# Kernel tuning notes

Hardware: AMD Instinct MI355X
Metric: run time of the kernel (lower is better)

The kernel has to match this reference:

```python
import jax, jax.numpy as jnp
import numpy as np


def setup_inputs() -> dict:
    key = jax.random.key(0)
    k1, k2 = jax.random.split(key)
    N, D, E = 8192, 4096, 16
    x = jax.random.normal(k1, (N, D), dtype=jnp.float32)
    Wg = jax.random.normal(k2, (E, D), dtype=jnp.float32) * (1.0 / np.sqrt(D))
    return {"x": x, "Wg": Wg, "k": 2}


def reference(x, Wg, k):
    # Router logits and gates (fp32, matching input.float() + Linear.float())
    logits = jnp.einsum("nd,ed->ne", x.astype(jnp.float32), Wg)  # [N, E]
    gates = jax.nn.softmax(logits, axis=1)
    N, E = gates.shape

    # top-k expert selection; concat column-wise like torch chunk(k, dim=1)
    _, topk_idx = jax.lax.top_k(gates, k)            # [N, k]
    idx = topk_idx.T.reshape(-1)                     # [k*N] token->expert

    # one-hot masks for each of the k choices, concatenated along token dim
    mask = jax.nn.one_hot(idx, E, dtype=jnp.int32)   # [k*N, E]

    # gate weights for each choice; normalize across the k=2 choices
    w_cols = jnp.take_along_axis(gates, topk_idx, axis=1)  # [N, k]
    w_norm = w_cols[:, 0] + w_cols[:, 1]
    weight = (w_cols / w_norm[:, None]).T.reshape(-1)      # [k*N]

    # expert token counts and within-expert positions (cumsum trick)
    expert_token_count = jnp.sum(mask, axis=0)                       # [E]
    pos_in_expert = jnp.sum((jnp.cumsum(mask, axis=0) - 1) * mask, axis=1)  # [k*N]

    # load-balancing aux loss uses only the top-1 mask
    me = jnp.mean(gates, axis=0)
    ce = jnp.mean(mask[:N].astype(jnp.float32), axis=0)
    l_aux = jnp.sum(me * ce) * E

    # exclusive cumsum of expert counts -> base offset per expert
    expert_offset = jnp.cumsum(expert_token_count) - expert_token_count
    token_pos_after = pos_in_expert + expert_offset[idx]             # [k*N]

    token_num = N * k
    token_pos_before = jnp.zeros((token_num,), dtype=jnp.int32).at[token_pos_after].set(
        jnp.arange(token_num, dtype=jnp.int32)
    )
    return (l_aux, token_pos_after, token_pos_before, expert_token_count, weight)
```

## Files before the change

kernel.cpp:

```cpp
#include <hip/hip_runtime.h>
#include <math.h>

#define N_TOK 8192
#define DIM   4096
#define NE    16
#define TOKS  (2*N_TOK)
#define NCHUNK (TOKS/64)
#define NSEG 4
#define SEGF4 (DIM/4/NSEG)
#define D4 (DIM/4)

#define OUT_LAUX 0
#define OUT_TPA  1
#define OUT_TPB  (1+TOKS)
#define OUT_CNT  (1+2*TOKS)
#define OUT_W    (1+2*TOKS+NE)

__global__ __launch_bounds__(256, 4) void k1_logits(
    const float4* __restrict__ x4, const float4* __restrict__ wg4,
    float* __restrict__ part)
{
    const int lane  = threadIdx.x & 63;
    const int wave  = threadIdx.x >> 6;
    const int gwave = blockIdx.x * 4 + wave;
    const int seg   = gwave & (NSEG - 1);
    const int row0  = (gwave >> 2) * 4;

    float acc[4][NE];
    #pragma unroll
    for (int r = 0; r < 4; ++r)
        #pragma unroll
        for (int e = 0; e < NE; ++e) acc[r][e] = 0.f;

    #pragma unroll 2
    for (int j = 0; j < SEGF4 / 64; ++j) {
        const int col = seg * SEGF4 + j * 64 + lane;
        float4 xv0 = x4[(size_t)(row0 + 0) * D4 + col];
        float4 xv1 = x4[(size_t)(row0 + 1) * D4 + col];
        float4 xv2 = x4[(size_t)(row0 + 2) * D4 + col];
        float4 xv3 = x4[(size_t)(row0 + 3) * D4 + col];
        #pragma unroll
        for (int e = 0; e < NE; ++e) {
            float4 wv = wg4[e * D4 + col];
            acc[0][e] = fmaf(xv0.x, wv.x, acc[0][e]);
            acc[0][e] = fmaf(xv0.y, wv.y, acc[0][e]);
            acc[0][e] = fmaf(xv0.z, wv.z, acc[0][e]);
            acc[0][e] = fmaf(xv0.w, wv.w, acc[0][e]);
            acc[1][e] = fmaf(xv1.x, wv.x, acc[1][e]);
            acc[1][e] = fmaf(xv1.y, wv.y, acc[1][e]);
            acc[1][e] = fmaf(xv1.z, wv.z, acc[1][e]);
            acc[1][e] = fmaf(xv1.w, wv.w, acc[1][e]);
            acc[2][e] = fmaf(xv2.x, wv.x, acc[2][e]);
            acc[2][e] = fmaf(xv2.y, wv.y, acc[2][e]);
            acc[2][e] = fmaf(xv2.z, wv.z, acc[2][e]);
            acc[2][e] = fmaf(xv2.w, wv.w, acc[2][e]);
            acc[3][e] = fmaf(xv3.x, wv.x, acc[3][e]);
            acc[3][e] = fmaf(xv3.y, wv.y, acc[3][e]);
            acc[3][e] = fmaf(xv3.z, wv.z, acc[3][e]);
            acc[3][e] = fmaf(xv3.w, wv.w, acc[3][e]);
        }
    }

    float v[64];
    #pragma unroll
    for (int r = 0; r < 4; ++r)
        #pragma unroll
        for (int e = 0; e < NE; ++e) v[r * 16 + e] = acc[r][e];

    #pragma unroll
    for (int s = 0; s < 6; ++s) {
        const int step = 1 << s;
        const int hi = (lane >> s) & 1;
        #pragma unroll
        for (int i = 0; i < (64 >> (s + 1)); ++i) {
            float a = v[2 * i], b = v[2 * i + 1];
            float mine = hi ? b : a;
            float oth  = hi ? a : b;
            v[i] = mine + __shfl_xor(oth, step);
        }
    }
    part[(size_t)seg * (N_TOK * NE) + (size_t)row0 * NE + lane] = v[0];
}

__global__ __launch_bounds__(256) void k2_route(
    const float* __restrict__ part, int* __restrict__ pr,
    int* __restrict__ hist, float* __restrict__ me_part,
    float* __restrict__ out)
{
    const int row   = blockIdx.x * 256 + threadIdx.x;
    const int lane  = threadIdx.x & 63;
    const int gwave = row >> 6;

    float lg[NE];
    #pragma unroll
    for (int e = 0; e < NE; ++e) lg[e] = 0.f;
    #pragma unroll
    for (int s = 0; s < NSEG; ++s) {
        const float4* p4 = (const float4*)(part + (size_t)s * (N_TOK * NE) + (size_t)row * NE);
        #pragma unroll
        for (int q = 0; q < 4; ++q) {
            float4 t = p4[q];
            lg[q * 4 + 0] += t.x;
            lg[q * 4 + 1] += t.y;
            lg[q * 4 + 2] += t.z;
            lg[q * 4 + 3] += t.w;
        }
    }

    float m1 = -INFINITY; int i1 = 0;
    #pragma unroll
    for (int e = 0; e < NE; ++e)
        if (lg[e] > m1) { m1 = lg[e]; i1 = e; }
    float m2 = -INFINITY; int i2 = 0;
    #pragma unroll
    for (int e = 0; e < NE; ++e)
        if (e != i1 && lg[e] > m2) { m2 = lg[e]; i2 = e; }

    float ssum = 0.f, ex[NE];
    #pragma unroll
    for (int e = 0; e < NE; ++e) { ex[e] = __expf(lg[e] - m1); ssum += ex[e]; }
    const float inv = 1.f / ssum;

    const float e2v = __expf(m2 - m1);
    const float w1  = 1.f / (1.f + e2v);
    out[OUT_W + row]         = w1;
    out[OUT_W + N_TOK + row] = 1.f - w1;

    float mymev = 0.f;
    #pragma unroll
    for (int e = 0; e < NE; ++e) {
        float mv = ex[e] * inv;
        mv += __shfl_xor(mv, 32); mv += __shfl_xor(mv, 16);
        mv += __shfl_xor(mv, 8);  mv += __shfl_xor(mv, 4);
        mv += __shfl_xor(mv, 2);  mv += __shfl_xor(mv, 1);
        if (lane == e) mymev = mv;
    }
    if (lane < NE) me_part[gwave * NE + lane] = mymev;

    const unsigned long long mlt = (1ull << lane) - 1ull;
    int rk1 = 0, rk2 = 0;
    #pragma unroll
    for (int eo = 0; eo < NE; ++eo) {
        unsigned long long mA = __ballot(i1 == eo);
        unsigned long long mB = __ballot(i2 == eo);
        if (i1 == eo) rk1 = (int)__popcll(mA & mlt);
        if (i2 == eo) rk2 = (int)__popcll(mB & mlt);
        if (lane == eo) {
            hist[gwave * NE + eo]                 = (int)__popcll(mA);
            hist[(NCHUNK / 2 + gwave) * NE + eo]  = (int)__popcll(mB);
        }
    }
    pr[row]         = i1 | (rk1 << 8);
    pr[N_TOK + row] = i2 | (rk2 << 8);
}

__global__ __launch_bounds__(1024) void k3_scan(
    const int* __restrict__ hist, const float* __restrict__ me_part,
    int* __restrict__ base, float* __restrict__ out)
{
    __shared__ int   sh[NCHUNK][NE];
    __shared__ int   counts[NE];
    __shared__ int   offs[NE];
    __shared__ int   ce_cnt[NE];
    __shared__ float me_red[64][NE];

    const int tid  = threadIdx.x;
    const int lane = tid & 63;
    const int wave = tid >> 6;

    if (wave < NE) {
        const int ecol = wave;
        int carry = 0;
        #pragma unroll
        for (int cc = 0; cc < 4; ++cc) {
            const int c = cc * 64 + lane;
            int v = hist[c * NE + ecol];
            const int orig = v;
            #pragma unroll
            for (int off = 1; off < 64; off <<= 1) {
                int n = __shfl_up(v, off, 64);
                if (lane >= off) v += n;
            }
            const int excl = v - orig + carry;
            if (c == NCHUNK / 2) ce_cnt[ecol] = excl;
            sh[c][ecol] = excl;
            carry += __shfl(v, 63, 64);
        }
        if (lane == 0) counts[ecol] = carry;
    }
    __syncthreads();

    if (tid == 0) {
        int run = 0;
        for (int e = 0; e < NE; ++e) { offs[e] = run; run += counts[e]; }
    }
    {
        const int e = tid & 15, g = tid >> 4;
        me_red[g][e] = me_part[g * NE + e] + me_part[(g + 64) * NE + e];
    }
    __syncthreads();

    if (wave == 0 && lane < NE) {
        float me = 0.f;
        for (int g = 0; g < 64; ++g) me += me_red[g][lane];
        me *= (1.0f / N_TOK);
        const float ce = (float)ce_cnt[lane] * (1.0f / N_TOK);
        float la = me * ce * (float)NE;
        la += __shfl_xor(la, 8); la += __shfl_xor(la, 4);
        la += __shfl_xor(la, 2); la += __shfl_xor(la, 1);
        if (lane == 0) out[OUT_LAUX] = la;
        out[OUT_CNT + lane] = (float)counts[lane];
    }

    #pragma unroll
    for (int k = 0; k < (NCHUNK * NE) / 1024; ++k) {
        const int i = k * 1024 + tid;
        base[i] = ((const int*)sh)[i] + offs[i & 15];
    }
}

__global__ __launch_bounds__(256) void k4_place(
    const int* __restrict__ pr, const int* __restrict__ base,
    float* __restrict__ out)
{
    const int t  = blockIdx.x * 256 + threadIdx.x;
    const int v  = pr[t];
    const int e  = v & 255;
    const int rk = v >> 8;
    const int c  = t >> 6;
    const int pos = base[c * NE + e] + rk;
    out[OUT_TPA + t]   = (float)pos;
    out[OUT_TPB + pos] = (float)t;
}

extern "C" void kernel_launch(void* const* d_in, const int* in_sizes, int n_in,
                              void* d_out, int out_size, void* d_ws, size_t ws_size,
                              hipStream_t stream) {
    const float* x  = (const float*)d_in[0];
    const float* wg = (const float*)d_in[1];
    float* out = (float*)d_out;

    char* w = (char*)d_ws;
    float* part    = (float*)w;
    w += (size_t)NSEG * N_TOK * NE * sizeof(float);
    int* pr        = (int*)w;   w += TOKS * sizeof(int);
    int* hist      = (int*)w;   w += NCHUNK * NE * sizeof(int);
    int* base      = (int*)w;   w += NCHUNK * NE * sizeof(int);
    float* me_part = (float*)w;

    k1_logits<<<(N_TOK / 4) * NSEG / 4, 256, 0, stream>>>(
        (const float4*)x, (const float4*)wg, part);
    k2_route<<<N_TOK / 256, 256, 0, stream>>>(part, pr, hist, me_part, out);
    k3_scan<<<1, 1024, 0, stream>>>(hist, me_part, base, out);
    k4_place<<<TOKS / 256, 256, 0, stream>>>(pr, base, out);
}
```

Measured before the change: 248.3 us.

## Fuse scan into placement kernel, stagger column order, simplify logits reduction

```diff
diff --git a/kernel.cpp b/kernel.cpp
--- a/kernel.cpp
+++ b/kernel.cpp
@@ -6,9 +6,10 @@
 #define NE    16
 #define TOKS  (2*N_TOK)
 #define NCHUNK (TOKS/64)
-#define NSEG 4
-#define SEGF4 (DIM/4/NSEG)
-#define D4 (DIM/4)
+#define D4    (DIM/4)
+#define NSEG  4
+#define SEGF4 (D4/NSEG)
+#define JITER (SEGF4/64)
 
 #define OUT_LAUX 0
 #define OUT_TPA  1
@@ -16,15 +17,16 @@
 #define OUT_CNT  (1+2*TOKS)
 #define OUT_W    (1+2*TOKS+NE)
 
-__global__ __launch_bounds__(256, 4) void k1_logits(
+__global__ __launch_bounds__(256) void k1_logits(
     const float4* __restrict__ x4, const float4* __restrict__ wg4,
     float* __restrict__ part)
 {
     const int lane  = threadIdx.x & 63;
     const int wave  = threadIdx.x >> 6;
     const int gwave = blockIdx.x * 4 + wave;
-    const int seg   = gwave & (NSEG - 1);
+    const int seg   = gwave & 3;
     const int row0  = (gwave >> 2) * 4;
+    const int ph    = gwave & 3;
 
     float acc[4][NE];
     #pragma unroll
@@ -33,7 +35,8 @@
         for (int e = 0; e < NE; ++e) acc[r][e] = 0.f;
 
     #pragma unroll 2
-    for (int j = 0; j < SEGF4 / 64; ++j) {
+    for (int jj = 0; jj < JITER; ++jj) {
+        const int j   = (jj + ph) & (JITER - 1);
         const int col = seg * SEGF4 + j * 64 + lane;
         float4 xv0 = x4[(size_t)(row0 + 0) * D4 + col];
         float4 xv1 = x4[(size_t)(row0 + 1) * D4 + col];
@@ -41,7 +44,7 @@
         float4 xv3 = x4[(size_t)(row0 + 3) * D4 + col];
         #pragma unroll
         for (int e = 0; e < NE; ++e) {
-            float4 wv = wg4[e * D4 + col];
+            const float4 wv = wg4[e * D4 + col];
             acc[0][e] = fmaf(xv0.x, wv.x, acc[0][e]);
             acc[0][e] = fmaf(xv0.y, wv.y, acc[0][e]);
             acc[0][e] = fmaf(xv0.z, wv.z, acc[0][e]);
@@ -61,45 +64,47 @@
         }
     }
 
-    float v[64];
     #pragma unroll
     for (int r = 0; r < 4; ++r)
         #pragma unroll
-        for (int e = 0; e < NE; ++e) v[r * 16 + e] = acc[r][e];
-
-    #pragma unroll
-    for (int s = 0; s < 6; ++s) {
-        const int step = 1 << s;
-        const int hi = (lane >> s) & 1;
-        #pragma unroll
-        for (int i = 0; i < (64 >> (s + 1)); ++i) {
-            float a = v[2 * i], b = v[2 * i + 1];
-            float mine = hi ? b : a;
-            float oth  = hi ? a : b;
-            v[i] = mine + __shfl_xor(oth, step);
-        }
-    }
-    part[(size_t)seg * (N_TOK * NE) + (size_t)row0 * NE + lane] = v[0];
-}
-
-__global__ __launch_bounds__(256) void k2_route(
+        for (int e = 0; e < NE; ++e) {
+            float v = acc[r][e];
+            v += __shfl_xor(v, 32); v += __shfl_xor(v, 16);
+            v += __shfl_xor(v, 8);  v += __shfl_xor(v, 4);
+            v += __shfl_xor(v, 2);  v += __shfl_xor(v, 1);
+            acc[r][e] = v;
+        }
+
+    if (lane < 4) {
+        const int r = lane;
+        float4* p4 = (float4*)part;
+        const size_t base = ((size_t)seg * N_TOK + row0 + r) * 4;
+        p4[base + 0] = make_float4(acc[r][0],  acc[r][1],  acc[r][2],  acc[r][3]);
+        p4[base + 1] = make_float4(acc[r][4],  acc[r][5],  acc[r][6],  acc[r][7]);
+        p4[base + 2] = make_float4(acc[r][8],  acc[r][9],  acc[r][10], acc[r][11]);
+        p4[base + 3] = make_float4(acc[r][12], acc[r][13], acc[r][14], acc[r][15]);
+    }
+}
+
+__global__ __launch_bounds__(128) void k2_route(
     const float* __restrict__ part, int* __restrict__ pr,
     int* __restrict__ hist, float* __restrict__ me_part,
     float* __restrict__ out)
 {
-    const int row   = blockIdx.x * 256 + threadIdx.x;
+    const int row   = blockIdx.x * 128 + threadIdx.x;
     const int lane  = threadIdx.x & 63;
     const int gwave = row >> 6;
 
     float lg[NE];
     #pragma unroll
     for (int e = 0; e < NE; ++e) lg[e] = 0.f;
+    const float4* p4 = (const float4*)part;
     #pragma unroll
     for (int s = 0; s < NSEG; ++s) {
-        const float4* p4 = (const float4*)(part + (size_t)s * (N_TOK * NE) + (size_t)row * NE);
+        const size_t base = ((size_t)s * N_TOK + row) * 4;
         #pragma unroll
         for (int q = 0; q < 4; ++q) {
-            float4 t = p4[q];
+            float4 t = p4[base + q];
             lg[q * 4 + 0] += t.x;
             lg[q * 4 + 1] += t.y;
             lg[q * 4 + 2] += t.z;
@@ -146,91 +151,108 @@
         if (i1 == eo) rk1 = (int)__popcll(mA & mlt);
         if (i2 == eo) rk2 = (int)__popcll(mB & mlt);
         if (lane == eo) {
-            hist[gwave * NE + eo]                 = (int)__popcll(mA);
-            hist[(NCHUNK / 2 + gwave) * NE + eo]  = (int)__popcll(mB);
+            hist[gwave * NE + eo]                = (int)__popcll(mA);
+            hist[(NCHUNK / 2 + gwave) * NE + eo] = (int)__popcll(mB);
         }
     }
     pr[row]         = i1 | (rk1 << 8);
     pr[N_TOK + row] = i2 | (rk2 << 8);
 }
 
-__global__ __launch_bounds__(1024) void k3_scan(
-    const int* __restrict__ hist, const float* __restrict__ me_part,
-    int* __restrict__ base, float* __restrict__ out)
+__global__ __launch_bounds__(256) void k3_place(
+    const int* __restrict__ pr, const int* __restrict__ hist,
+    const float* __restrict__ me_part, float* __restrict__ out)
 {
-    __shared__ int   sh[NCHUNK][NE];
-    __shared__ int   counts[NE];
-    __shared__ int   offs[NE];
-    __shared__ int   ce_cnt[NE];
-    __shared__ float me_red[64][NE];
-
-    const int tid  = threadIdx.x;
-    const int lane = tid & 63;
-    const int wave = tid >> 6;
-
-    if (wave < NE) {
-        const int ecol = wave;
-        int carry = 0;
-        #pragma unroll
-        for (int cc = 0; cc < 4; ++cc) {
-            const int c = cc * 64 + lane;
-            int v = hist[c * NE + ecol];
-            const int orig = v;
+    __shared__ int   sh[NCHUNK][20];
+    __shared__ int   cnt_sh[NE], ce_sh[NE];
+    __shared__ float me_sh[16][17];
+    __shared__ float me_tot[NE];
+
+    const int t = threadIdx.x;
+
+    int h[NE];
+    {
+        const int4* h4 = (const int4*)(hist + t * NE);
+        int4 a = h4[0], b = h4[1], c = h4[2], d = h4[3];
+        h[0]=a.x; h[1]=a.y; h[2]=a.z; h[3]=a.w;
+        h[4]=b.x; h[5]=b.y; h[6]=b.z; h[7]=b.w;
+        h[8]=c.x; h[9]=c.y; h[10]=c.z; h[11]=c.w;
+        h[12]=d.x; h[13]=d.y; h[14]=d.z; h[15]=d.w;
+    }
+    #pragma unroll
+    for (int e = 0; e < NE; ++e) sh[t][e] = h[e];
+    __syncthreads();
+
+    for (int off = 1; off < NCHUNK; off <<= 1) {
+        int tmp[NE];
+        #pragma unroll
+        for (int e = 0; e < NE; ++e) tmp[e] = (t >= off) ? sh[t - off][e] : 0;
+        __syncthreads();
+        #pragma unroll
+        for (int e = 0; e < NE; ++e) sh[t][e] += tmp[e];
+        __syncthreads();
+    }
+
+    if (t == NCHUNK - 1) {
+        #pragma unroll
+        for (int e = 0; e < NE; ++e) cnt_sh[e] = sh[t][e];
+    }
+    if (t == NCHUNK / 2 - 1) {
+        #pragma unroll
+        for (int e = 0; e < NE; ++e) ce_sh[e] = sh[t][e];
+    }
+
+    int ex[NE];
+    #pragma unroll
+    for (int e = 0; e < NE; ++e) ex[e] = sh[t][e] - h[e];
+    __syncthreads();
+    #pragma unroll
+    for (int e = 0; e < NE; ++e) sh[t][e] = ex[e];
+    __syncthreads();
+
+    int offs[NE];
+    {
+        int run = 0;
+        #pragma unroll
+        for (int e = 0; e < NE; ++e) { offs[e] = run; run += cnt_sh[e]; }
+    }
+
+    {
+        const int tk = blockIdx.x * 256 + t;
+        const int v  = pr[tk];
+        const int e  = v & 255;
+        const int rk = v >> 8;
+        const int c  = tk >> 6;
+        const int pos = sh[c][e] + offs[e] + rk;
+        out[OUT_TPA + tk]  = (float)pos;
+        out[OUT_TPB + pos] = (float)tk;
+    }
+
+    if (blockIdx.x == 0) {
+        {
+            const int e = t & 15, g = t >> 4;
+            float s = 0.f;
             #pragma unroll
-            for (int off = 1; off < 64; off <<= 1) {
-                int n = __shfl_up(v, off, 64);
-                if (lane >= off) v += n;
-            }
-            const int excl = v - orig + carry;
-            if (c == NCHUNK / 2) ce_cnt[ecol] = excl;
-            sh[c][ecol] = excl;
-            carry += __shfl(v, 63, 64);
-        }
-        if (lane == 0) counts[ecol] = carry;
-    }
-    __syncthreads();
-
-    if (tid == 0) {
-        int run = 0;
-        for (int e = 0; e < NE; ++e) { offs[e] = run; run += counts[e]; }
-    }
-    {
-        const int e = tid & 15, g = tid >> 4;
-        me_red[g][e] = me_part[g * NE + e] + me_part[(g + 64) * NE + e];
-    }
-    __syncthreads();
-
-    if (wave == 0 && lane < NE) {
-        float me = 0.f;
-        for (int g = 0; g < 64; ++g) me += me_red[g][lane];
-        me *= (1.0f / N_TOK);
-        const float ce = (float)ce_cnt[lane] * (1.0f / N_TOK);
-        float la = me * ce * (float)NE;
-        la += __shfl_xor(la, 8); la += __shfl_xor(la, 4);
-        la += __shfl_xor(la, 2); la += __shfl_xor(la, 1);
-        if (lane == 0) out[OUT_LAUX] = la;
-        out[OUT_CNT + lane] = (float)counts[lane];
-    }
-
-    #pragma unroll
-    for (int k = 0; k < (NCHUNK * NE) / 1024; ++k) {
-        const int i = k * 1024 + tid;
-        base[i] = ((const int*)sh)[i] + offs[i & 15];
-    }
-}
-
-__global__ __launch_bounds__(256) void k4_place(
-    const int* __restrict__ pr, const int* __restrict__ base,
-    float* __restrict__ out)
-{
-    const int t  = blockIdx.x * 256 + threadIdx.x;
-    const int v  = pr[t];
-    const int e  = v & 255;
-    const int rk = v >> 8;
-    const int c  = t >> 6;
-    const int pos = base[c * NE + e] + rk;
-    out[OUT_TPA + t]   = (float)pos;
-    out[OUT_TPB + pos] = (float)t;
+            for (int k = 0; k < 8; ++k) s += me_part[(g + 16 * k) * NE + e];
+            me_sh[g][e] = s;
+        }
+        __syncthreads();
+        if (t < NE) {
+            float me = 0.f;
+            #pragma unroll
+            for (int g = 0; g < 16; ++g) me += me_sh[g][t];
+            me_tot[t] = me;
+            out[OUT_CNT + t] = (float)cnt_sh[t];
+        }
+        __syncthreads();
+        if (t == 0) {
+            float la = 0.f;
+            #pragma unroll
+            for (int e = 0; e < NE; ++e)
+                la += (me_tot[e] * (1.0f / N_TOK)) * ((float)ce_sh[e] * (1.0f / N_TOK));
+            out[OUT_LAUX] = la * (float)NE;
+        }
+    }
 }
 
 extern "C" void kernel_launch(void* const* d_in, const int* in_sizes, int n_in,
@@ -241,16 +263,13 @@
     float* out = (float*)d_out;
 
     char* w = (char*)d_ws;
-    float* part    = (float*)w;
-    w += (size_t)NSEG * N_TOK * NE * sizeof(float);
-    int* pr        = (int*)w;   w += TOKS * sizeof(int);
-    int* hist      = (int*)w;   w += NCHUNK * NE * sizeof(int);
-    int* base      = (int*)w;   w += NCHUNK * NE * sizeof(int);
+    float* part    = (float*)w;  w += (size_t)NSEG * N_TOK * NE * sizeof(float);
+    int*   pr      = (int*)w;    w += TOKS * sizeof(int);
+    int*   hist    = (int*)w;    w += NCHUNK * NE * sizeof(int);
     float* me_part = (float*)w;
 
     k1_logits<<<(N_TOK / 4) * NSEG / 4, 256, 0, stream>>>(
         (const float4*)x, (const float4*)wg, part);
-    k2_route<<<N_TOK / 256, 256, 0, stream>>>(part, pr, hist, me_part, out);
-    k3_scan<<<1, 1024, 0, stream>>>(hist, me_part, base, out);
-    k4_place<<<TOKS / 256, 256, 0, stream>>>(pr, base, out);
-}
+    k2_route<<<N_TOK / 128, 128, 0, stream>>>(part, pr, hist, me_part, out);
+    k3_place<<<TOKS / 256, 256, 0, stream>>>(pr, hist, me_part, out);
+}
```

Result: slower. 269.5 us (+8.5%).
